# Kernel tuning notes

Measured on AMD Instinct MI355X. Metric: run time of the kernel, lower is better.

Reference implementation:

```python
import jax, jax.numpy as jnp
import numpy as np

LAYER_BS = 63
N_SITES = 12
B = 2048


def _kaiming_uniform(key, shape, fan_in):
    # torch kaiming_uniform_ with a=0: bound = sqrt(6/fan_in)
    bound = np.sqrt(6.0 / fan_in)
    return jax.random.uniform(key, shape, jnp.float32, -bound, bound)


def _cnn12(x, w):
    # x: (B, L, 12, Cin); w: (L, 3*Cin, Cout)
    nn0 = jnp.roll(x, -1, axis=-2) + jnp.roll(x, 3, axis=-2)
    nnn0 = jnp.roll(x, -2, axis=-2) + jnp.roll(x, 4, axis=-2)
    c0 = jnp.concatenate([nn0, nnn0], axis=-1)          # (B,L,12,2*Cin)
    c1 = c0 + jnp.roll(c0, -2, axis=-2)
    allc = jnp.concatenate([x, c1], axis=-1)            # (B,L,12,3*Cin)
    return jnp.einsum('blsc,lco->blso', allc, w)


def _batch_linear(x, w, b):
    # x: (B, L, F); w: (L, F, O); b: (L, O)
    return jnp.einsum('blf,lfo->blo', x, w) + b


def setup_inputs() -> dict:
    key = jax.random.key(0)
    ks = jax.random.split(key, 9)
    zs = jax.random.normal(ks[0], (B, LAYER_BS, N_SITES, 2), jnp.float32)
    # CNN weights: (L, 3*Cin, Cout); kaiming fan_in = 3*Cin
    w1 = _kaiming_uniform(ks[1], (LAYER_BS, 6, 32), 6)
    w2 = _kaiming_uniform(ks[2], (LAYER_BS, 96, 64), 96)
    fw1 = _kaiming_uniform(ks[3], (LAYER_BS, 128, 64), 128)
    fb1 = jax.random.uniform(ks[4], (LAYER_BS, 64), jnp.float32, -1 / np.sqrt(128), 1 / np.sqrt(128))
    fw2 = _kaiming_uniform(ks[5], (LAYER_BS, 64, 64), 64)
    fb2 = jax.random.uniform(ks[6], (LAYER_BS, 64), jnp.float32, -1 / np.sqrt(64), 1 / np.sqrt(64))
    fw3 = _kaiming_uniform(ks[7], (LAYER_BS, 64, 1), 64)
    fb3 = jax.random.uniform(ks[8], (LAYER_BS, 1), jnp.float32, -1 / np.sqrt(64), 1 / np.sqrt(64))
    return {"zs": zs, "w1": w1, "w2": w2, "fw1": fw1, "fb1": fb1,
            "fw2": fw2, "fb2": fb2, "fw3": fw3, "fb3": fb3}


def reference(zs, w1, w2, fw1, fb1, fw2, fb2, fw3, fb3):
    h = jax.nn.relu(_cnn12(zs, w1))                     # (B,L,12,32)
    h = jax.nn.relu(_cnn12(h, w2))                      # (B,L,12,64)
    h = jnp.concatenate([h.mean(axis=-2), h.max(axis=-2)], axis=-1)
    h = jax.nn.relu(_batch_linear(h, fw1, fb1))
    h = jax.nn.relu(_batch_linear(h, fw2, fb2))
    out = _batch_linear(h, fw3, fb3)                    # (B,L,1)
    return out[..., 0]                                  # (B,L)
```

## Files before the change

kernel.cpp:

```cpp
#include <hip/hip_runtime.h>


#define LNUM 63
#define BT 16
#define NBT 128
#define WSL 19968

typedef __attribute__((ext_vector_type(8))) _Float16 half8;
typedef __attribute__((ext_vector_type(2))) _Float16 half2v;
typedef __attribute__((ext_vector_type(4))) float floatx4;
typedef __attribute__((ext_vector_type(4))) unsigned uint4v;

static __device__ __forceinline__ unsigned cvtpk(float a, float b) {
    return __builtin_bit_cast(unsigned, __builtin_amdgcn_cvt_pkrtz(a, b));
}
static __device__ __forceinline__ half2v u2h(unsigned u) { return __builtin_bit_cast(half2v, u); }
static __device__ __forceinline__ float hlo16(unsigned short s) {
    return (float)__builtin_bit_cast(_Float16, s);
}
static __device__ __forceinline__ int w12(int v) { return v >= 12 ? v - 12 : v; }
static __device__ __forceinline__ float2 add2(float2 a, float2 b) { return make_float2(a.x + b.x, a.y + b.y); }

#define O_POOLDW 3072
#define O_POOLUS 6144
#define O_POOL2  0
#define O_G2     1280

__global__ void prep(const float* __restrict__ w2, const float* __restrict__ fw1,
                     const float* __restrict__ fw2, unsigned short* __restrict__ ws) {
    __shared__ float S[8192];
    const int l = blockIdx.x, r = blockIdx.y, t = threadIdx.x;
    if (r == 0) {
        const float4* src = (const float4*)(w2 + (size_t)l * 6144);
        #pragma unroll
        for (int j = 0; j < 6; ++j) *(float4*)(S + 4 * (t + 256 * j)) = src[t + 256 * j];
        __syncthreads();
        unsigned* dst = (unsigned*)(ws + (size_t)l * WSL);
        #pragma unroll
        for (int j = 0; j < 13; ++j) {
            int i = j * 256 + t, o = i / 52, cp = i - 52 * o, c = 2 * cp;
            dst[i] = cvtpk(S[c * 64 + o], S[c * 64 + 64 + o]);
        }
    } else if (r == 1) {
        const float4* src = (const float4*)(fw1 + (size_t)l * 8192);
        #pragma unroll
        for (int j = 0; j < 8; ++j) *(float4*)(S + 4 * (t + 256 * j)) = src[t + 256 * j];
        __syncthreads();
        unsigned* dst = (unsigned*)(ws + (size_t)l * WSL + 6656);
        #pragma unroll
        for (int j = 0; j < 17; ++j) {
            int i = j * 256 + t, o = i / 68, cp = i - 68 * o;
            dst[i] = cvtpk(S[cp * 64 + o], S[(64 + cp) * 64 + o]);
        }
    } else {
        const float4* src = (const float4*)(fw2 + (size_t)l * 4096);
        #pragma unroll
        for (int j = 0; j < 4; ++j) *(float4*)(S + 4 * (t + 256 * j)) = src[t + 256 * j];
        __syncthreads();
        unsigned* dst = (unsigned*)(ws + (size_t)l * WSL + 15360);
        #pragma unroll
        for (int j = 0; j < 9; ++j) {
            int i = j * 256 + t, o = i / 36, cp = i - 36 * o, c = 2 * cp;
            dst[i] = cvtpk(S[c * 64 + o], S[c * 64 + 64 + o]);
        }
    }
}

__global__ __launch_bounds__(256, 4) void fused_nn(
    const float* __restrict__ zs,  const float* __restrict__ w1,
    const float* __restrict__ fb1, const float* __restrict__ fb2,
    const float* __restrict__ fw3, const float* __restrict__ fb3,
    const unsigned short* __restrict__ ws,
    float* __restrict__ out)
{
    __shared__ __align__(16) unsigned U[4160];
    unsigned short* USH = (unsigned short*)U;

    const int t    = threadIdx.x;
    const int lane = t & 63;
    const int wv   = t >> 6;
    const int n    = lane & 15;
    const int quad = lane >> 4;
    const int l    = blockIdx.x / NBT;
    const int b0   = (blockIdx.x % NBT) * BT;

    uint4v bwp[3][4];
    {
        const uint4v* w2q = (const uint4v*)(ws + (size_t)l * WSL);
        #pragma unroll
        for (int ks = 0; ks < 3; ++ks)
            #pragma unroll
            for (int nt = 0; nt < 4; ++nt)
                bwp[ks][nt] = w2q[(nt * 16 + n) * 13 + ks * 4 + quad];
    }

    {
        const int b = t >> 4, cpair = t & 15, c0 = cpair * 2;
        const float* xb = zs + ((size_t)(b0 + b) * LNUM + l) * 24;
        float4 xq[6];
        #pragma unroll
        for (int q = 0; q < 6; ++q) xq[q] = *(const float4*)(xb + q * 4);
        float2 xv[12], xr[12], xA[12], xB[12];
        #pragma unroll
        for (int s = 0; s < 12; ++s)
            xv[s] = (s & 1) ? make_float2(xq[s >> 1].z, xq[s >> 1].w)
                            : make_float2(xq[s >> 1].x, xq[s >> 1].y);
        #pragma unroll
        for (int s = 0; s < 12; ++s) xr[s] = add2(xv[w12(s + 1)], xv[w12(s + 11)]);
        #pragma unroll
        for (int s = 0; s < 12; ++s) {
            xA[s] = add2(xr[w12(s + 2)], xr[w12(s + 10)]);
            xB[s] = add2(xr[w12(s + 3)], xr[w12(s + 9)]);
        }
        const float* wl = w1 + (size_t)l * 192 + c0;
        const float2 w0  = *(const float2*)(wl);
        const float2 w1v = *(const float2*)(wl + 32);
        const float2 w2v = *(const float2*)(wl + 64);
        const float2 w3v = *(const float2*)(wl + 96);
        const float2 w4v = *(const float2*)(wl + 128);
        const float2 w5v = *(const float2*)(wl + 160);
        #pragma unroll
        for (int s = 0; s < 12; ++s) {
            float hx = xv[s].x*w0.x + xv[s].y*w1v.x + xA[s].x*w2v.x + xA[s].y*w3v.x
                     + xB[s].x*w4v.x + xB[s].y*w5v.x;
            float hy = xv[s].x*w0.y + xv[s].y*w1v.y + xA[s].x*w2v.y + xA[s].y*w3v.y
                     + xB[s].x*w4v.y + xB[s].y*w5v.y;
            U[(b * 12 + s) * 20 + cpair] = cvtpk(fmaxf(hx, 0.f), fmaxf(hy, 0.f));
        }
    }
    const float bias1 = fb1[(size_t)l * 64 + wv * 16 + n];
    const float bias2 = fb2[(size_t)l * 64 + wv * 16 + n];
    __syncthreads();

    floatx4 acc[3][4];
    #pragma unroll
    for (int mi = 0; mi < 3; ++mi)
        #pragma unroll
        for (int nt = 0; nt < 4; ++nt) acc[mi][nt] = (floatx4){0.f, 0.f, 0.f, 0.f};
    {
        int bi[3], si[3];
        #pragma unroll
        for (int mi = 0; mi < 3; ++mi) {
            int row = 48 * wv + 16 * mi + n;
            bi[mi] = row / 12;
            si[mi] = row - 12 * bi[mi];
        }
        const int q4 = quad * 4;
        const int dA[4] = {1, 11, 3, 9};
        const int dB[4] = {2, 10, 4, 8};
        #pragma unroll
        for (int ks = 0; ks < 3; ++ks) {
            half8 af[3];
            #pragma unroll
            for (int mi = 0; mi < 3; ++mi) {
                const int rb = bi[mi] * 12, s = si[mi];
                if (ks == 0) {
                    af[mi] = *(const half8*)(U + (rb + s) * 20 + q4);
                } else {
                    const int* d = (ks == 1) ? dA : dB;
                    half8 l0 = *(const half8*)(U + (rb + w12(s + d[0])) * 20 + q4);
                    half8 l1 = *(const half8*)(U + (rb + w12(s + d[1])) * 20 + q4);
                    half8 l2 = *(const half8*)(U + (rb + w12(s + d[2])) * 20 + q4);
                    half8 l3 = *(const half8*)(U + (rb + w12(s + d[3])) * 20 + q4);
                    af[mi] = (l0 + l1) + (l2 + l3);
                }
            }
            #pragma unroll
            for (int mi = 0; mi < 3; ++mi)
                #pragma unroll
                for (int nt = 0; nt < 4; ++nt)
                    acc[mi][nt] = __builtin_amdgcn_mfma_f32_16x16x32_f16(
                        af[mi], __builtin_bit_cast(half8, bwp[ks][nt]), acc[mi][nt], 0, 0, 0);
        }
    }
    __syncthreads();

    #pragma unroll
    for (int mi = 0; mi < 3; ++mi) {
        const int rr = 48 * wv + 16 * mi + 4 * quad;
        const int bq = rr / 12;
        const int chk = (rr - 12 * bq) >> 2;
        #pragma unroll
        for (int nt = 0; nt < 4; ++nt) {
            const int ch = nt * 16 + n;
            float r0 = fmaxf(acc[mi][nt][0], 0.f), r1 = fmaxf(acc[mi][nt][1], 0.f);
            float r2 = fmaxf(acc[mi][nt][2], 0.f), r3 = fmaxf(acc[mi][nt][3], 0.f);
            float sm = (r0 + r1) + (r2 + r3);
            float mx = fmaxf(fmaxf(r0, r1), fmaxf(r2, r3));
            U[(bq * 64 + ch) * 3 + chk] = cvtpk(sm, mx);
        }
    }
    __builtin_amdgcn_wave_barrier();

    {
        const unsigned* p = U + t * 12;
        uint4v q0 = *(const uint4v*)(p);
        uint4v q1 = *(const uint4v*)(p + 4);
        uint4v q2 = *(const uint4v*)(p + 8);
        unsigned arr[12] = {q0.x, q0.y, q0.z, q0.w, q1.x, q1.y, q1.z, q1.w,
                            q2.x, q2.y, q2.z, q2.w};
        const int b = t >> 4, ch0 = (t * 4) & 63;
        const _Float16 inv12 = (_Float16)(1.0f / 12.0f);
        unsigned pk[4];
        #pragma unroll
        for (int j = 0; j < 4; ++j) {
            half2v d0 = u2h(arr[3 * j]), d1 = u2h(arr[3 * j + 1]), d2 = u2h(arr[3 * j + 2]);
            _Float16 s = (d0[0] + d1[0]) + d2[0];
            _Float16 m0 = d0[1] > d1[1] ? d0[1] : d1[1];
            _Float16 m  = m0 > d2[1] ? m0 : d2[1];
            half2v pm;
            pm[0] = s * inv12;
            pm[1] = m;
            pk[j] = __builtin_bit_cast(unsigned, pm);
        }
        uint2 w01 = make_uint2(pk[0], pk[1]), w23 = make_uint2(pk[2], pk[3]);
        *(uint2*)(U + O_POOLDW + b * 68 + ch0)     = w01;
        *(uint2*)(U + O_POOLDW + b * 68 + ch0 + 2) = w23;
    }
    __syncthreads();

    {
        const int o = wv * 16 + n;
        floatx4 a1 = (floatx4){bias1, bias1, bias1, bias1};
        const uint4v* f1q = (const uint4v*)(ws + (size_t)l * WSL + 6656);
        #pragma unroll
        for (int ks = 0; ks < 4; ++ks) {
            half8 av = *(const half8*)(USH + O_POOLUS + n * 136 + ks * 32 + quad * 8);
            uint4v bw = f1q[o * 17 + ks * 4 + quad];
            a1 = __builtin_amdgcn_mfma_f32_16x16x32_f16(av, __builtin_bit_cast(half8, bw), a1, 0, 0, 0);
        }
        #pragma unroll
        for (int i = 0; i < 2; ++i) {
            unsigned pk = cvtpk(fmaxf(a1[2 * i], 0.f), fmaxf(a1[2 * i + 1], 0.f));
            USH[O_POOL2 + (quad * 4 + 2 * i)     * 72 + o] = (unsigned short)(pk & 0xffffu);
            USH[O_POOL2 + (quad * 4 + 2 * i + 1) * 72 + o] = (unsigned short)(pk >> 16);
        }
    }
    __syncthreads();

    {
        const int o = wv * 16 + n;
        floatx4 a2 = (floatx4){bias2, bias2, bias2, bias2};
        const uint4v* f2q = (const uint4v*)(ws + (size_t)l * WSL + 15360);
        #pragma unroll
        for (int ks = 0; ks < 2; ++ks) {
            half8 av = *(const half8*)(USH + O_POOL2 + n * 72 + ks * 32 + quad * 8);
            uint4v bw = f2q[o * 9 + ks * 4 + quad];
            a2 = __builtin_amdgcn_mfma_f32_16x16x32_f16(av, __builtin_bit_cast(half8, bw), a2, 0, 0, 0);
        }
        #pragma unroll
        for (int i = 0; i < 2; ++i) {
            unsigned pk = cvtpk(fmaxf(a2[2 * i], 0.f), fmaxf(a2[2 * i + 1], 0.f));
            USH[O_G2 + (quad * 4 + 2 * i)     * 72 + o] = (unsigned short)(pk & 0xffffu);
            USH[O_G2 + (quad * 4 + 2 * i + 1) * 72 + o] = (unsigned short)(pk >> 16);
        }
    }
    __syncthreads();

    if (t < 16) {
        float a = fb3[l];
        const float* w3 = fw3 + (size_t)l * 64;
        #pragma unroll
        for (int c4 = 0; c4 < 16; ++c4) {
            uint2 u2 = *(const uint2*)(USH + O_G2 + t * 72 + c4 * 4);
            float4 w = *(const float4*)(w3 + c4 * 4);
            a += hlo16((unsigned short)(u2.x & 0xffff)) * w.x
               + hlo16((unsigned short)(u2.x >> 16))    * w.y
               + hlo16((unsigned short)(u2.y & 0xffff)) * w.z
               + hlo16((unsigned short)(u2.y >> 16))    * w.w;
        }
        out[(size_t)(b0 + t) * LNUM + l] = a;
    }
}

extern "C" void kernel_launch(void* const* d_in, const int* in_sizes, int n_in,
                              void* d_out, int out_size, void* d_ws, size_t ws_size,
                              hipStream_t stream) {
    const float* zs  = (const float*)d_in[0];
    const float* w1  = (const float*)d_in[1];
    const float* w2  = (const float*)d_in[2];
    const float* fw1 = (const float*)d_in[3];
    const float* fb1 = (const float*)d_in[4];
    const float* fw2 = (const float*)d_in[5];
    const float* fb2 = (const float*)d_in[6];
    const float* fw3 = (const float*)d_in[7];
    const float* fb3 = (const float*)d_in[8];
    float* out = (float*)d_out;
    unsigned short* ws = (unsigned short*)d_ws;

    hipLaunchKernelGGL(prep, dim3(LNUM, 3), dim3(256), 0, stream, w2, fw1, fw2, ws);
    hipLaunchKernelGGL(fused_nn, dim3(LNUM * NBT), dim3(256), 0, stream,
                       zs, w1, fb1, fb2, fw3, fb3, ws, out);
}
```

Baseline: 134.2 us.

## Stage conv2 weights in LDS and split tap sums into separate MFMAs

Copies the per-layer fp16 conv2 weights into shared memory with coalesced loads instead of holding 48 registers of weights per thread. Conv2 now issues one MFMA per neighbour tap (9 taps) rather than summing four half8 loads before each MFMA, which also avoids fp16 adds. Conv1 neighbour sums are computed inline to cut register arrays, and launch bounds are raised to 5 blocks per CU. The trade-off is three times as many MFMAs, a larger LDS footprint per block, and extra LDS traffic for weights.

```diff
diff --git a/kernel.cpp b/kernel.cpp
--- a/kernel.cpp
+++ b/kernel.cpp
@@ -21,6 +21,7 @@
 static __device__ __forceinline__ int w12(int v) { return v >= 12 ? v - 12 : v; }
 static __device__ __forceinline__ float2 add2(float2 a, float2 b) { return make_float2(a.x + b.x, a.y + b.y); }
 
+#define O_W2DW   4160
 #define O_POOLDW 3072
 #define O_POOLUS 6144
 #define O_POOL2  0
@@ -66,14 +67,14 @@
     }
 }
 
-__global__ __launch_bounds__(256, 4) void fused_nn(
+__global__ __launch_bounds__(256, 5) void fused_nn(
     const float* __restrict__ zs,  const float* __restrict__ w1,
     const float* __restrict__ fb1, const float* __restrict__ fb2,
     const float* __restrict__ fw3, const float* __restrict__ fb3,
     const unsigned short* __restrict__ ws,
     float* __restrict__ out)
 {
-    __shared__ __align__(16) unsigned U[4160];
+    __shared__ __align__(16) unsigned U[7488];
     unsigned short* USH = (unsigned short*)U;
 
     const int t    = threadIdx.x;
@@ -84,33 +85,28 @@
     const int l    = blockIdx.x / NBT;
     const int b0   = (blockIdx.x % NBT) * BT;
 
-    uint4v bwp[3][4];
-    {
-        const uint4v* w2q = (const uint4v*)(ws + (size_t)l * WSL);
-        #pragma unroll
-        for (int ks = 0; ks < 3; ++ks)
-            #pragma unroll
-            for (int nt = 0; nt < 4; ++nt)
-                bwp[ks][nt] = w2q[(nt * 16 + n) * 13 + ks * 4 + quad];
+    {
+        const uint4v* src = (const uint4v*)(ws + (size_t)l * WSL);
+        uint4v s0 = src[t];
+        uint4v s1 = src[t + 256];
+        uint4v s2 = src[t + 512];
+        uint4v s3 = (t < 64) ? src[t + 768] : (uint4v){0, 0, 0, 0};
+        uint4v* dst = (uint4v*)(U + O_W2DW);
+        dst[t]       = s0;
+        dst[t + 256] = s1;
+        dst[t + 512] = s2;
+        if (t < 64) dst[t + 768] = s3;
     }
 
     {
         const int b = t >> 4, cpair = t & 15, c0 = cpair * 2;
         const float* xb = zs + ((size_t)(b0 + b) * LNUM + l) * 24;
-        float4 xq[6];
-        #pragma unroll
-        for (int q = 0; q < 6; ++q) xq[q] = *(const float4*)(xb + q * 4);
-        float2 xv[12], xr[12], xA[12], xB[12];
-        #pragma unroll
-        for (int s = 0; s < 12; ++s)
-            xv[s] = (s & 1) ? make_float2(xq[s >> 1].z, xq[s >> 1].w)
-                            : make_float2(xq[s >> 1].x, xq[s >> 1].y);
-        #pragma unroll
-        for (int s = 0; s < 12; ++s) xr[s] = add2(xv[w12(s + 1)], xv[w12(s + 11)]);
-        #pragma unroll
-        for (int s = 0; s < 12; ++s) {
-            xA[s] = add2(xr[w12(s + 2)], xr[w12(s + 10)]);
-            xB[s] = add2(xr[w12(s + 3)], xr[w12(s + 9)]);
+        float2 xv[12];
+        #pragma unroll
+        for (int q = 0; q < 6; ++q) {
+            float4 xq = *(const float4*)(xb + q * 4);
+            xv[2 * q]     = make_float2(xq.x, xq.y);
+            xv[2 * q + 1] = make_float2(xq.z, xq.w);
         }
         const float* wl = w1 + (size_t)l * 192 + c0;
         const float2 w0  = *(const float2*)(wl);
@@ -121,10 +117,14 @@
         const float2 w5v = *(const float2*)(wl + 160);
         #pragma unroll
         for (int s = 0; s < 12; ++s) {
-            float hx = xv[s].x*w0.x + xv[s].y*w1v.x + xA[s].x*w2v.x + xA[s].y*w3v.x
-                     + xB[s].x*w4v.x + xB[s].y*w5v.x;
-            float hy = xv[s].x*w0.y + xv[s].y*w1v.y + xA[s].x*w2v.y + xA[s].y*w3v.y
-                     + xB[s].x*w4v.y + xB[s].y*w5v.y;
+            float2 xA = add2(add2(xv[w12(s + 1)], xv[w12(s + 11)]),
+                             add2(xv[w12(s + 3)], xv[w12(s + 9)]));
+            float2 xB = add2(add2(xv[w12(s + 2)], xv[w12(s + 10)]),
+                             add2(xv[w12(s + 4)], xv[w12(s + 8)]));
+            float hx = xv[s].x*w0.x + xv[s].y*w1v.x + xA.x*w2v.x + xA.y*w3v.x
+                     + xB.x*w4v.x + xB.y*w5v.x;
+            float hy = xv[s].x*w0.y + xv[s].y*w1v.y + xA.x*w2v.y + xA.y*w3v.y
+                     + xB.x*w4v.y + xB.y*w5v.y;
             U[(b * 12 + s) * 20 + cpair] = cvtpk(fmaxf(hx, 0.f), fmaxf(hy, 0.f));
         }
     }
@@ -138,39 +138,40 @@
         #pragma unroll
         for (int nt = 0; nt < 4; ++nt) acc[mi][nt] = (floatx4){0.f, 0.f, 0.f, 0.f};
     {
-        int bi[3], si[3];
+        int rbq[3], a20[3];
         #pragma unroll
         for (int mi = 0; mi < 3; ++mi) {
             int row = 48 * wv + 16 * mi + n;
-            bi[mi] = row / 12;
-            si[mi] = row - 12 * bi[mi];
-        }
-        const int q4 = quad * 4;
-        const int dA[4] = {1, 11, 3, 9};
-        const int dB[4] = {2, 10, 4, 8};
-        #pragma unroll
-        for (int ks = 0; ks < 3; ++ks) {
+            int bi = row / 12;
+            int si = row - 12 * bi;
+            rbq[mi] = bi * 240 + quad * 4;
+            a20[mi] = si * 20;
+        }
+        const uint4v* w2l = (const uint4v*)(U + O_W2DW);
+        const int c13 = n * 13 + quad;
+        constexpr int tapd[9] = {0, 1, 11, 3, 9, 2, 10, 4, 8};
+        uint4v bw[4];
+        #pragma unroll
+        for (int i = 0; i < 9; ++i) {
+            const int sec = (i == 0) ? 0 : (i < 5 ? 1 : 2);
+            if (i == 0 || i == 1 || i == 5) {
+                #pragma unroll
+                for (int nt = 0; nt < 4; ++nt)
+                    bw[nt] = w2l[c13 + nt * 208 + sec * 4];
+            }
             half8 af[3];
             #pragma unroll
             for (int mi = 0; mi < 3; ++mi) {
-                const int rb = bi[mi] * 12, s = si[mi];
-                if (ks == 0) {
-                    af[mi] = *(const half8*)(U + (rb + s) * 20 + q4);
-                } else {
-                    const int* d = (ks == 1) ? dA : dB;
-                    half8 l0 = *(const half8*)(U + (rb + w12(s + d[0])) * 20 + q4);
-                    half8 l1 = *(const half8*)(U + (rb + w12(s + d[1])) * 20 + q4);
-                    half8 l2 = *(const half8*)(U + (rb + w12(s + d[2])) * 20 + q4);
-                    half8 l3 = *(const half8*)(U + (rb + w12(s + d[3])) * 20 + q4);
-                    af[mi] = (l0 + l1) + (l2 + l3);
-                }
+                int off = a20[mi] + tapd[i] * 20;
+                if (tapd[i]) { if (off >= 240) off -= 240; }
+                af[mi] = *(const half8*)(U + rbq[mi] + off);
             }
             #pragma unroll
             for (int mi = 0; mi < 3; ++mi)
                 #pragma unroll
                 for (int nt = 0; nt < 4; ++nt)
                     acc[mi][nt] = __builtin_amdgcn_mfma_f32_16x16x32_f16(
-                        af[mi], __builtin_bit_cast(half8, bwp[ks][nt]), acc[mi][nt], 0, 0, 0);
+                        af[mi], __builtin_bit_cast(half8, bw[nt]), acc[mi][nt], 0, 0, 0);
         }
     }
     __syncthreads();
```

New measurement: 146.6 us. 9.3% more time.

## Compute first conv layer with MFMA via prepacked circulant weights; stage w2 in LDS

Applied to the files above, without the earlier changes.

The first 12-site convolution, previously scalar FP32 per thread with register-level neighbour sums, becomes an MFMA. Prep builds a circulant fp16 weight matrix that folds the neighbour-shift structure into a (12*32)x24 operand, and each wave multiplies it against fp16-converted inputs. The second-layer weights are now copied cooperatively into LDS and read per k-step, instead of being held in 48 registers per thread. This cuts VALU work and register pressure but grows LDS use per block (about 28KB), which may limit occupancy, and it converts inputs to fp16 earlier, lowering precision.

```diff
diff --git a/kernel.cpp b/kernel.cpp
--- a/kernel.cpp
+++ b/kernel.cpp
@@ -4,7 +4,7 @@
 #define LNUM 63
 #define BT 16
 #define NBT 128
-#define WSL 19968
+#define WSL 29184
 
 typedef __attribute__((ext_vector_type(8))) _Float16 half8;
 typedef __attribute__((ext_vector_type(2))) _Float16 half2v;
@@ -19,15 +19,16 @@
     return (float)__builtin_bit_cast(_Float16, s);
 }
 static __device__ __forceinline__ int w12(int v) { return v >= 12 ? v - 12 : v; }
-static __device__ __forceinline__ float2 add2(float2 a, float2 b) { return make_float2(a.x + b.x, a.y + b.y); }
-
+
+#define O_H1     3328
 #define O_POOLDW 3072
 #define O_POOLUS 6144
 #define O_POOL2  0
 #define O_G2     1280
 
 __global__ void prep(const float* __restrict__ w2, const float* __restrict__ fw1,
-                     const float* __restrict__ fw2, unsigned short* __restrict__ ws) {
+                     const float* __restrict__ fw2, const float* __restrict__ w1,
+                     unsigned short* __restrict__ ws) {
     __shared__ float S[8192];
     const int l = blockIdx.x, r = blockIdx.y, t = threadIdx.x;
     if (r == 0) {
@@ -52,7 +53,7 @@
             int i = j * 256 + t, o = i / 68, cp = i - 68 * o;
             dst[i] = cvtpk(S[cp * 64 + o], S[(64 + cp) * 64 + o]);
         }
-    } else {
+    } else if (r == 2) {
         const float4* src = (const float4*)(fw2 + (size_t)l * 4096);
         #pragma unroll
         for (int j = 0; j < 4; ++j) *(float4*)(S + 4 * (t + 256 * j)) = src[t + 256 * j];
@@ -62,6 +63,22 @@
         for (int j = 0; j < 9; ++j) {
             int i = j * 256 + t, o = i / 36, cp = i - 36 * o, c = 2 * cp;
             dst[i] = cvtpk(S[c * 64 + o], S[c * 64 + 64 + o]);
+        }
+    } else {
+        if (t < 192) S[t] = w1[(size_t)l * 192 + t];
+        __syncthreads();
+        unsigned* dst = (unsigned*)(ws + (size_t)l * WSL + 19968);
+        #pragma unroll
+        for (int j = 0; j < 18; ++j) {
+            int i = j * 256 + t;
+            int row = i / 12, kp = i - 12 * row;
+            int s = row >> 5, o = row & 31;
+            int d = kp - s; if (d < 0) d += 12;
+            unsigned v = 0;
+            if (d == 0)                                    v = cvtpk(S[o],       S[32 + o]);
+            else if (d == 1 || d == 3 || d == 9 || d == 11) v = cvtpk(S[64 + o],  S[96 + o]);
+            else if (d == 2 || d == 4 || d == 8 || d == 10) v = cvtpk(S[128 + o], S[160 + o]);
+            dst[i] = v;
         }
     }
 }
@@ -73,7 +90,7 @@
     const unsigned short* __restrict__ ws,
     float* __restrict__ out)
 {
-    __shared__ __align__(16) unsigned U[4160];
+    __shared__ __align__(16) unsigned U[7168];
     unsigned short* USH = (unsigned short*)U;
 
     const int t    = threadIdx.x;
@@ -84,48 +101,46 @@
     const int l    = blockIdx.x / NBT;
     const int b0   = (blockIdx.x % NBT) * BT;
 
-    uint4v bwp[3][4];
-    {
-        const uint4v* w2q = (const uint4v*)(ws + (size_t)l * WSL);
-        #pragma unroll
-        for (int ks = 0; ks < 3; ++ks)
-            #pragma unroll
-            for (int nt = 0; nt < 4; ++nt)
-                bwp[ks][nt] = w2q[(nt * 16 + n) * 13 + ks * 4 + quad];
-    }
-
-    {
-        const int b = t >> 4, cpair = t & 15, c0 = cpair * 2;
-        const float* xb = zs + ((size_t)(b0 + b) * LNUM + l) * 24;
-        float4 xq[6];
-        #pragma unroll
-        for (int q = 0; q < 6; ++q) xq[q] = *(const float4*)(xb + q * 4);
-        float2 xv[12], xr[12], xA[12], xB[12];
-        #pragma unroll
-        for (int s = 0; s < 12; ++s)
-            xv[s] = (s & 1) ? make_float2(xq[s >> 1].z, xq[s >> 1].w)
-                            : make_float2(xq[s >> 1].x, xq[s >> 1].y);
-        #pragma unroll
-        for (int s = 0; s < 12; ++s) xr[s] = add2(xv[w12(s + 1)], xv[w12(s + 11)]);
-        #pragma unroll
-        for (int s = 0; s < 12; ++s) {
-            xA[s] = add2(xr[w12(s + 2)], xr[w12(s + 10)]);
-            xB[s] = add2(xr[w12(s + 3)], xr[w12(s + 9)]);
-        }
-        const float* wl = w1 + (size_t)l * 192 + c0;
-        const float2 w0  = *(const float2*)(wl);
-        const float2 w1v = *(const float2*)(wl + 32);
-        const float2 w2v = *(const float2*)(wl + 64);
-        const float2 w3v = *(const float2*)(wl + 96);
-        const float2 w4v = *(const float2*)(wl + 128);
-        const float2 w5v = *(const float2*)(wl + 160);
-        #pragma unroll
-        for (int s = 0; s < 12; ++s) {
-            float hx = xv[s].x*w0.x + xv[s].y*w1v.x + xA[s].x*w2v.x + xA[s].y*w3v.x
-                     + xB[s].x*w4v.x + xB[s].y*w5v.x;
-            float hy = xv[s].x*w0.y + xv[s].y*w1v.y + xA[s].x*w2v.y + xA[s].y*w3v.y
-                     + xB[s].x*w4v.y + xB[s].y*w5v.y;
-            U[(b * 12 + s) * 20 + cpair] = cvtpk(fmaxf(hx, 0.f), fmaxf(hy, 0.f));
+    {
+        const uint4v* src = (const uint4v*)(ws + (size_t)l * WSL);
+        uint4v s0 = src[t];
+        uint4v s1 = src[t + 256];
+        uint4v s2 = src[t + 512];
+        uint4v* dst = (uint4v*)U;
+        if (t < 64) {
+            uint4v s3 = src[t + 768];
+            dst[t] = s0; dst[t + 256] = s1; dst[t + 512] = s2; dst[t + 768] = s3;
+        } else {
+            dst[t] = s0; dst[t + 256] = s1; dst[t + 512] = s2;
+        }
+    }
+
+    half8 xb;
+    {
+        uint4v z = {0u, 0u, 0u, 0u};
+        if (quad < 3) {
+            const float* xr = zs + ((size_t)(b0 + n) * LNUM + l) * 24 + quad * 8;
+            float4 x0 = *(const float4*)(xr);
+            float4 x1 = *(const float4*)(xr + 4);
+            z.x = cvtpk(x0.x, x0.y); z.y = cvtpk(x0.z, x0.w);
+            z.z = cvtpk(x1.x, x1.y); z.w = cvtpk(x1.z, x1.w);
+        }
+        xb = __builtin_bit_cast(half8, z);
+    }
+    {
+        const uint4v* wbt = (const uint4v*)(ws + (size_t)l * WSL + 19968);
+        #pragma unroll
+        for (int i = 0; i < 6; ++i) {
+            const int rt = 6 * wv + i;
+            uint4v au = {0u, 0u, 0u, 0u};
+            if (quad < 3) au = wbt[(rt * 16 + n) * 3 + quad];
+            floatx4 c = __builtin_amdgcn_mfma_f32_16x16x32_f16(
+                __builtin_bit_cast(half8, au), xb, (floatx4){0.f, 0.f, 0.f, 0.f}, 0, 0, 0);
+            unsigned pk0 = cvtpk(fmaxf(c[0], 0.f), fmaxf(c[1], 0.f));
+            unsigned pk1 = cvtpk(fmaxf(c[2], 0.f), fmaxf(c[3], 0.f));
+            const int s = rt >> 1;
+            const int dwoff = (rt & 1) * 8 + 2 * quad;
+            *(uint2*)(U + O_H1 + (n * 12 + s) * 20 + dwoff) = make_uint2(pk0, pk1);
         }
     }
     const float bias1 = fb1[(size_t)l * 64 + wv * 16 + n];
@@ -138,30 +153,37 @@
         #pragma unroll
         for (int nt = 0; nt < 4; ++nt) acc[mi][nt] = (floatx4){0.f, 0.f, 0.f, 0.f};
     {
-        int bi[3], si[3];
+        int rb_[3], si_[3];
         #pragma unroll
         for (int mi = 0; mi < 3; ++mi) {
             int row = 48 * wv + 16 * mi + n;
-            bi[mi] = row / 12;
-            si[mi] = row - 12 * bi[mi];
-        }
+            int bi = row / 12;
+            si_[mi] = row - 12 * bi;
+            rb_[mi] = bi * 12;
+        }
+        const uint4v* w2l = (const uint4v*)U;
+        const int c13 = n * 13 + quad;
         const int q4 = quad * 4;
         const int dA[4] = {1, 11, 3, 9};
         const int dB[4] = {2, 10, 4, 8};
         #pragma unroll
         for (int ks = 0; ks < 3; ++ks) {
+            uint4v bw[4];
+            #pragma unroll
+            for (int nt = 0; nt < 4; ++nt)
+                bw[nt] = w2l[c13 + nt * 208 + ks * 4];
             half8 af[3];
             #pragma unroll
             for (int mi = 0; mi < 3; ++mi) {
-                const int rb = bi[mi] * 12, s = si[mi];
+                const int rb = rb_[mi], s = si_[mi];
                 if (ks == 0) {
-                    af[mi] = *(const half8*)(U + (rb + s) * 20 + q4);
+                    af[mi] = *(const half8*)(U + O_H1 + (rb + s) * 20 + q4);
                 } else {
                     const int* d = (ks == 1) ? dA : dB;
-                    half8 l0 = *(const half8*)(U + (rb + w12(s + d[0])) * 20 + q4);
-                    half8 l1 = *(const half8*)(U + (rb + w12(s + d[1])) * 20 + q4);
-                    half8 l2 = *(const half8*)(U + (rb + w12(s + d[2])) * 20 + q4);
-                    half8 l3 = *(const half8*)(U + (rb + w12(s + d[3])) * 20 + q4);
+                    half8 l0 = *(const half8*)(U + O_H1 + (rb + w12(s + d[0])) * 20 + q4);
+                    half8 l1 = *(const half8*)(U + O_H1 + (rb + w12(s + d[1])) * 20 + q4);
+                    half8 l2 = *(const half8*)(U + O_H1 + (rb + w12(s + d[2])) * 20 + q4);
+                    half8 l3 = *(const half8*)(U + O_H1 + (rb + w12(s + d[3])) * 20 + q4);
                     af[mi] = (l0 + l1) + (l2 + l3);
                 }
             }
@@ -170,7 +192,7 @@
                 #pragma unroll
                 for (int nt = 0; nt < 4; ++nt)
                     acc[mi][nt] = __builtin_amdgcn_mfma_f32_16x16x32_f16(
-                        af[mi], __builtin_bit_cast(half8, bwp[ks][nt]), acc[mi][nt], 0, 0, 0);
+                        af[mi], __builtin_bit_cast(half8, bw[nt]), acc[mi][nt], 0, 0, 0);
         }
     }
     __syncthreads();
@@ -288,7 +310,7 @@
     float* out = (float*)d_out;
     unsigned short* ws = (unsigned short*)d_ws;
 
-    hipLaunchKernelGGL(prep, dim3(LNUM, 3), dim3(256), 0, stream, w2, fw1, fw2, ws);
+    hipLaunchKernelGGL(prep, dim3(LNUM, 4), dim3(256), 0, stream, w2, fw1, fw2, w1, ws);
     hipLaunchKernelGGL(fused_nn, dim3(LNUM * NBT), dim3(256), 0, stream,
                        zs, w1, fb1, fb2, fw3, fb3, ws, out);
 }
```

Result: slower. 146.8 us (+9.4%).
